# Performance work log

Hardware: AMD Instinct MI355X
Metric: run time of the kernel (lower is better)

The kernel has to match this reference:

```python
import jax, jax.numpy as jnp
import numpy as np

B, N_O, N_Q = 2, 512, 512
POS_DIM, LATENT, HEADS, HEAD_DIM, OUT_DIM = 3, 256, 8, 32, 128
HD = HEADS * HEAD_DIM  # == LATENT here


def _lin(key, fan_in, fan_out):
    return jax.random.normal(key, (fan_in, fan_out), jnp.float32) / np.sqrt(fan_in)


def setup_inputs() -> dict:
    key = jax.random.key(0)
    ks = jax.random.split(key, 12)
    return {
        'h_obs': jax.random.normal(ks[0], (B, N_O, LATENT), jnp.float32),
        'pos_obs': jax.random.uniform(ks[1], (B, N_O, POS_DIM), jnp.float32),
        'pos_query': jax.random.uniform(ks[2], (B, N_Q, POS_DIM), jnp.float32),
        'fw1': _lin(ks[3], LATENT, LATENT), 'fb1': jnp.zeros((LATENT,), jnp.float32),
        'fw2': _lin(ks[4], LATENT, HD), 'fb2': jnp.zeros((HD,), jnp.float32),
        'log_sigma': jnp.zeros((HEADS,), jnp.float32),
        'kw1': _lin(ks[5], POS_DIM * 3, LATENT), 'kb1': jnp.zeros((LATENT,), jnp.float32),
        'kw2': _lin(ks[6], LATENT, HEADS), 'kb2': jnp.zeros((HEADS,), jnp.float32),
        'ow': _lin(ks[7], HD, OUT_DIM), 'ob': jnp.zeros((OUT_DIM,), jnp.float32),
        'vw': _lin(ks[8], HD, OUT_DIM), 'vb': jnp.zeros((OUT_DIM,), jnp.float32),
    }


def reference(h_obs, pos_obs, pos_query, fw1, fb1, fw2, fb2, log_sigma,
              kw1, kb1, kw2, kb2, ow, ob, vw, vb):
    Bv, No, _ = h_obs.shape
    Nq = pos_query.shape[1]
    # feature net -> values [B, H, N_o, D]
    v = jax.nn.relu(h_obs @ fw1 + fb1) @ fw2 + fb2
    v = v.reshape(Bv, No, HEADS, HEAD_DIM).transpose(0, 2, 1, 3)
    # pairwise relative positions [B, Nq, No, P]
    pos_q = pos_query[:, :, None, :]
    pos_o = pos_obs[:, None, :, :]
    rel = pos_q - pos_o
    dist2 = jnp.sum(rel ** 2, axis=-1)  # [B, Nq, No]
    sigma = jnp.exp(log_sigma)[None, :, None, None]
    rbf = jnp.exp(-dist2[:, None] / (sigma ** 2 + 1e-6))  # [B, H, Nq, No]
    # kernel MLP on concatenated pairwise positions [B, Nq, No, 3P] -> [B, H, Nq, No]
    ki = jnp.concatenate([
        jnp.broadcast_to(pos_q, (Bv, Nq, No, POS_DIM)),
        jnp.broadcast_to(pos_o, (Bv, Nq, No, POS_DIM)),
        rel], axis=-1)
    delta = (jax.nn.relu(ki @ kw1 + kb1) @ kw2 + kb2).transpose(0, 3, 1, 2)
    logits = jnp.log(rbf + 1e-8) + delta
    weights = jax.nn.softmax(logits, axis=-1)  # [B, H, Nq, No]
    # weighted mean over observations
    v_mean = jnp.einsum('bhqo,bhod->bhqd', weights, v)  # [B, H, Nq, D]
    h_query = v_mean.transpose(0, 2, 1, 3).reshape(Bv, Nq, HD)
    # weighted variance: sum_o w * (v_o - v_mean)^2
    residual = v[:, :, None, :, :] - v_mean[:, :, :, None, :]  # [B, H, Nq, No, D]
    var = jnp.sum(weights[..., None] * residual ** 2, axis=3)  # [B, H, Nq, D]
    var = var.transpose(0, 2, 1, 3).reshape(Bv, Nq, HD)
    mean = h_query @ ow + ob
    var_out = jax.nn.softplus(var @ vw + vb)
    return (mean, var_out)
```

## Files before the change

### kernel.cpp

```cpp
#include <hip/hip_runtime.h>
#include <math.h>

#define NB 2
#define NO 512
#define NQ 512
#define OUT_DIM 128
#define LPAD 516

typedef __attribute__((ext_vector_type(8))) _Float16 half8;
typedef __attribute__((ext_vector_type(4))) _Float16 half4;
typedef __attribute__((ext_vector_type(4))) float f32x4;

__device__ __forceinline__ float softplus_f(float x) {
  return x > 0.0f ? x + log1pf(expf(-x)) : log1pf(expf(x));
}
__device__ __forceinline__ half8 splat8(_Float16 v) {
  return (half8){v, v, v, v, v, v, v, v};
}
__device__ __forceinline__ half8 fma8(half8 a, half8 b, half8 c) {
  return __builtin_elementwise_fma(a, b, c);
}
__device__ __forceinline__ half8 max8(half8 a, half8 b) {
  return __builtin_elementwise_max(a, b);
}
__device__ __forceinline__ void gll16(const void* g, void* l) {
  __builtin_amdgcn_global_load_lds(
      (const __attribute__((address_space(1))) unsigned int*)g,
      (__attribute__((address_space(3))) unsigned int*)l, 16, 0, 0);
}

__global__ __launch_bounds__(1024) void prep_kernel(
    const float* __restrict__ h_obs, const float* __restrict__ fw1,
    const float* __restrict__ fb1, const float* __restrict__ fw2,
    const float* __restrict__ fb2, _Float16* __restrict__ VT)
{
  __shared__ float s_red[4][4][256];
  __shared__ float s_hid[4][256];
  const int n  = threadIdx.x & 255;
  const int ks = threadIdx.x >> 8;
  const int r0 = blockIdx.x * 4;
  const int k0 = ks * 64;
  float a0 = 0.f, a1 = 0.f, a2 = 0.f, a3 = 0.f;
  #pragma unroll 8
  for (int kk = 0; kk < 64; ++kk) {
    int k = k0 + kk;
    float w = fw1[k * 256 + n];
    a0 = fmaf(h_obs[(r0 + 0) * 256 + k], w, a0);
    a1 = fmaf(h_obs[(r0 + 1) * 256 + k], w, a1);
    a2 = fmaf(h_obs[(r0 + 2) * 256 + k], w, a2);
    a3 = fmaf(h_obs[(r0 + 3) * 256 + k], w, a3);
  }
  s_red[ks][0][n] = a0; s_red[ks][1][n] = a1;
  s_red[ks][2][n] = a2; s_red[ks][3][n] = a3;
  __syncthreads();
  if (ks == 0) {
    float bb = fb1[n];
    #pragma unroll
    for (int r = 0; r < 4; ++r) {
      float v = s_red[0][r][n] + s_red[1][r][n] + s_red[2][r][n] + s_red[3][r][n] + bb;
      s_hid[r][n] = fmaxf(v, 0.f);
    }
  }
  __syncthreads();
  float c0 = 0.f, c1 = 0.f, c2 = 0.f, c3 = 0.f;
  #pragma unroll 8
  for (int kk = 0; kk < 64; ++kk) {
    int k = k0 + kk;
    float w = fw2[k * 256 + n];
    c0 = fmaf(s_hid[0][k], w, c0);
    c1 = fmaf(s_hid[1][k], w, c1);
    c2 = fmaf(s_hid[2][k], w, c2);
    c3 = fmaf(s_hid[3][k], w, c3);
  }
  __syncthreads();
  s_red[ks][0][n] = c0; s_red[ks][1][n] = c1;
  s_red[ks][2][n] = c2; s_red[ks][3][n] = c3;
  __syncthreads();
  if (ks == 0) {
    float bb = fb2[n];
    float vr[4];
    #pragma unroll
    for (int r = 0; r < 4; ++r)
      vr[r] = s_red[0][r][n] + s_red[1][r][n] + s_red[2][r][n] + s_red[3][r][n] + bb;
    const int h  = n >> 5, d = n & 31;
    const int bb_ = r0 >> 9, o0 = r0 & 511;
    half4 pv;
    #pragma unroll
    for (int r = 0; r < 4; ++r) pv[r] = (_Float16)vr[r];
    *(half4*)(VT + ((size_t)((bb_ * 8 + h) * 32 + d)) * 512 + o0) = pv;
  }
}

__global__ __launch_bounds__(512, 4) void attn_fused(
    const _Float16* __restrict__ VT,
    const float* __restrict__ kw1,
    const float* __restrict__ kb1,
    const float* __restrict__ kw2,
    const float* __restrict__ kb2,
    const float* __restrict__ log_sigma,
    const float* __restrict__ pos_obs,
    const float* __restrict__ pos_query,
    const float* __restrict__ ow, const float* __restrict__ obias,
    const float* __restrict__ vw, const float* __restrict__ vbias,
    float* __restrict__ out)
{
  __shared__ __align__(16) float s_logits[2][8 * LPAD];
  __shared__ __align__(16) _Float16 s_P16[2][8][520];
  __shared__ half8 s_Bh[512];
  __shared__ __align__(16) float s_pool[2048];
  __shared__ __align__(16) float s_po[3][516];
  __shared__ __align__(16) _Float16 s_co[3][264];

  _Float16* s_aq2 = (_Float16*)s_pool;
  float*    s_hv   = s_pool;
  float*    s_pred = s_pool + 1024;

  const int t   = threadIdx.x;
  const int bq0 = blockIdx.x * 2;
  const int b   = bq0 >> 9;

  float pqx[2], pqy[2], pqz[2];
  #pragma unroll
  for (int q = 0; q < 2; ++q) {
    pqx[q] = pos_query[(bq0 + q) * 3 + 0];
    pqy[q] = pos_query[(bq0 + q) * 3 + 1];
    pqz[q] = pos_query[(bq0 + q) * 3 + 2];
  }
  {
    const int q = t >> 8, j = t & 255;
    float c0 = kw1[0 * 256 + j] + kw1[6 * 256 + j];
    float c1 = kw1[1 * 256 + j] + kw1[7 * 256 + j];
    float c2 = kw1[2 * 256 + j] + kw1[8 * 256 + j];
    s_aq2[q * 256 + j] = (_Float16)
        fmaf(pqx[q], c0, fmaf(pqy[q], c1, fmaf(pqz[q], c2, kb1[j])));
  }
  if (t < 256) {
    const int j = t;
    s_co[0][j] = (_Float16)(kw1[3 * 256 + j] - kw1[6 * 256 + j]);
    s_co[1][j] = (_Float16)(kw1[4 * 256 + j] - kw1[7 * 256 + j]);
    s_co[2][j] = (_Float16)(kw1[5 * 256 + j] - kw1[8 * 256 + j]);
  }
  {
    const int o = t;
    const float* p = pos_obs + (size_t)(b * NO + o) * 3;
    float px = p[0], py = p[1], pz = p[2];
    s_po[0][o] = px; s_po[1][o] = py; s_po[2][o] = pz;
    float d2q[2];
    #pragma unroll
    for (int q = 0; q < 2; ++q) {
      float r0 = pqx[q] - px, r1 = pqy[q] - py, r2 = pqz[q] - pz;
      d2q[q] = r0 * r0 + r1 * r1 + r2 * r2;
    }
    #pragma unroll
    for (int h = 0; h < 8; ++h) {
      float sg  = __expf(log_sigma[h]);
      float inv = 1.0f / (sg * sg + 1e-6f);
      float kbv = kb2[h];
      s_logits[0][h * LPAD + o] = __logf(__expf(-d2q[0] * inv) + 1e-8f) + kbv;
      s_logits[1][h * LPAD + o] = __logf(__expf(-d2q[1] * inv) + 1e-8f) + kbv;
    }
  }
  {
    const int kstep = t >> 6, lane = t & 63;
    const int nh = lane & 15;
    const int kb_ = kstep * 32 + ((lane >> 4) & 3) * 8;
    half8 b8;
    #pragma unroll
    for (int i = 0; i < 8; ++i) {
      float v = (nh < 8) ? kw2[(kb_ + i) * 8 + nh] : 0.f;
      b8[i] = (_Float16)v;
    }
    s_Bh[kstep * 64 + lane] = b8;
  }
  __syncthreads();

  {
    const int wave = t >> 6, lane = t & 63;
    const int quad = lane >> 4, mrow = lane & 15;
    const int tb   = wave * 4;
    _Float16 pxh[4], pyh[4], pzh[4];
    #pragma unroll
    for (int jt = 0; jt < 4; ++jt) {
      const int o = (tb + jt) * 16 + mrow;
      pxh[jt] = (_Float16)s_po[0][o];
      pyh[jt] = (_Float16)s_po[1][o];
      pzh[jt] = (_Float16)s_po[2][o];
    }
    f32x4 C[2][4];
    #pragma unroll
    for (int q = 0; q < 2; ++q)
      #pragma unroll
      for (int jt = 0; jt < 4; ++jt) C[q][jt] = (f32x4){0.f, 0.f, 0.f, 0.f};

    const half8 z8 = {0, 0, 0, 0, 0, 0, 0, 0};
    #pragma unroll
    for (int kstep = 0; kstep < 8; ++kstep) {
      const int koff = kstep * 32 + quad * 8;
      half8 c0 = *(const half8*)&s_co[0][koff];
      half8 c1 = *(const half8*)&s_co[1][koff];
      half8 c2 = *(const half8*)&s_co[2][koff];
      half8 aq0 = *(const half8*)(s_aq2 + koff);
      half8 aq1 = *(const half8*)(s_aq2 + 256 + koff);
      half8 bh  = s_Bh[kstep * 64 + lane];
      #pragma unroll
      for (int jt = 0; jt < 4; ++jt) {
        half8 ao = fma8(splat8(pxh[jt]), c0,
                   fma8(splat8(pyh[jt]), c1, splat8(pzh[jt]) * c2));
        half8 a0 = max8(aq0 + ao, z8);
        half8 a1 = max8(aq1 + ao, z8);
        C[0][jt] = __builtin_amdgcn_mfma_f32_16x16x32_f16(a0, bh, C[0][jt], 0, 0, 0);
        C[1][jt] = __builtin_amdgcn_mfma_f32_16x16x32_f16(a1, bh, C[1][jt], 0, 0, 0);
      }
    }
    const int hh = lane & 15;
    if (hh < 8) {
      #pragma unroll
      for (int q = 0; q < 2; ++q)
        #pragma unroll
        for (int jt = 0; jt < 4; ++jt) {
          const int ob2 = (tb + jt) * 16 + quad * 4;
          #pragma unroll
          for (int r = 0; r < 4; ++r)
            s_logits[q][hh * LPAD + ob2 + r] += C[q][jt][r];
        }
    }
  }
  __syncthreads();

  {
    const int h = t >> 6, lane = t & 63;
    float invq[2];
    #pragma unroll
    for (int q = 0; q < 2; ++q) {
      float* pl = &s_logits[q][h * LPAD];
      float l8[8];
      float m = -1e30f;
      #pragma unroll
      for (int k = 0; k < 8; ++k) {
        l8[k] = pl[k * 64 + lane];
        m = fmaxf(m, l8[k]);
      }
      #pragma unroll
      for (int off = 32; off >= 1; off >>= 1) m = fmaxf(m, __shfl_xor(m, off, 64));
      float s = 0.f;
      #pragma unroll
      for (int k = 0; k < 8; ++k) {
        float p = __expf(l8[k] - m);
        s += p;
        s_P16[q][h][k * 64 + lane] = (_Float16)p;
      }
      #pragma unroll
      for (int off = 32; off >= 1; off >>= 1) s += __shfl_xor(s, off, 64);
      invq[q] = 1.0f / s;
    }
    __syncthreads();

    const int kg = lane >> 4, dl = lane & 15;
    char* stg = (char*)s_logits + h * 4096;
    const _Float16* vt = VT + ((size_t)(b * 8 + h) << 14);
    const _Float16* vsrc = vt + (lane >> 1) * 512 + (lane & 1) * 8;
    #define STAGE(j) gll16(vsrc + (j) * 16, stg + ((j) & 3) * 1024)
    STAGE(0); STAGE(1); STAGE(2); STAGE(3);

    const _Float16* pB = &s_P16[lane & 1][h][0];
    f32x4 Cm0 = {0.f, 0.f, 0.f, 0.f}, Cm1 = Cm0, Cv0 = Cm0, Cv1 = Cm0;
    #pragma unroll
    for (int ks = 0; ks < 16; ++ks) {
      if (ks < 15) asm volatile("s_waitcnt vmcnt(2)" ::: "memory");
      else         asm volatile("s_waitcnt vmcnt(0)" ::: "memory");
      const char* bufc = stg + ((2 * ks + (kg >> 1)) & 3) * 1024
                       + dl * 32 + (kg & 1) * 16;
      half8 am0 = *(const half8*)(bufc);
      half8 am1 = *(const half8*)(bufc + 512);
      half8 pb  = *(const half8*)(pB + ks * 32 + kg * 8);
      half8 av0 = am0 * am0;
      half8 av1 = am1 * am1;
      Cm0 = __builtin_amdgcn_mfma_f32_16x16x32_f16(am0, pb, Cm0, 0, 0, 0);
      Cm1 = __builtin_amdgcn_mfma_f32_16x16x32_f16(am1, pb, Cm1, 0, 0, 0);
      Cv0 = __builtin_amdgcn_mfma_f32_16x16x32_f16(av0, pb, Cv0, 0, 0, 0);
      Cv1 = __builtin_amdgcn_mfma_f32_16x16x32_f16(av1, pb, Cv1, 0, 0, 0);
      if (ks < 14) {
        asm volatile("s_waitcnt lgkmcnt(0)" ::: "memory");
        STAGE(2 * ks + 4); STAGE(2 * ks + 5);
      }
    }
    #undef STAGE
    const int nq = lane & 15;
    if (nq < 2) {
      const float iv = invq[nq];
      const int dbase = h * 32 + kg * 4;
      f32x4 m0, v0, m1, v1;
      #pragma unroll
      for (int r = 0; r < 4; ++r) {
        float a = Cm0[r] * iv;
        m0[r] = a; v0[r] = fmaxf(Cv0[r] * iv - a * a, 0.f);
        float c = Cm1[r] * iv;
        m1[r] = c; v1[r] = fmaxf(Cv1[r] * iv - c * c, 0.f);
      }
      *(f32x4*)(s_hv + (nq * 2 + 0) * 256 + dbase)      = m0;
      *(f32x4*)(s_hv + (nq * 2 + 1) * 256 + dbase)      = v0;
      *(f32x4*)(s_hv + (nq * 2 + 0) * 256 + dbase + 16) = m1;
      *(f32x4*)(s_hv + (nq * 2 + 1) * 256 + dbase + 16) = v1;
    }
  }
  __syncthreads();

  {
    const int ks = t >> 8, mode = (t >> 7) & 1, n = t & 127;
    const float* W  = mode ? vw : ow;
    const float* X0 = s_hv + mode * 256;
    const float* X1 = s_hv + (2 + mode) * 256;
    float a0 = 0.f, a1 = 0.f;
    const int k0 = ks * 128;
    #pragma unroll 4
    for (int k = k0; k < k0 + 128; k += 4) {
      float4 x0 = *(const float4*)&X0[k];
      float4 x1 = *(const float4*)&X1[k];
      float w0 = W[(k + 0) * 128 + n];
      float w1 = W[(k + 1) * 128 + n];
      float w2 = W[(k + 2) * 128 + n];
      float w3 = W[(k + 3) * 128 + n];
      a0 = fmaf(x0.x, w0, a0); a1 = fmaf(x1.x, w0, a1);
      a0 = fmaf(x0.y, w1, a0); a1 = fmaf(x1.y, w1, a1);
      a0 = fmaf(x0.z, w2, a0); a1 = fmaf(x1.z, w2, a1);
      a0 = fmaf(x0.w, w3, a0); a1 = fmaf(x1.w, w3, a1);
    }
    s_pred[((ks * 2 + mode) * 2 + 0) * 128 + n] = a0;
    s_pred[((ks * 2 + mode) * 2 + 1) * 128 + n] = a1;
  }
  __syncthreads();
  {
    const int q = t >> 8, mode = (t >> 7) & 1, n = t & 127;
    float v = s_pred[((0 * 2 + mode) * 2 + q) * 128 + n]
            + s_pred[((1 * 2 + mode) * 2 + q) * 128 + n]
            + (mode ? vbias[n] : obias[n]);
    if (mode) v = softplus_f(v);
    out[(size_t)mode * (NB * NQ * OUT_DIM) + (size_t)(bq0 + q) * OUT_DIM + n] = v;
  }
}

extern "C" void kernel_launch(void* const* d_in, const int* in_sizes, int n_in,
                              void* d_out, int out_size, void* d_ws, size_t ws_size,
                              hipStream_t stream)
{
  const float* h_obs     = (const float*)d_in[0];
  const float* pos_obs   = (const float*)d_in[1];
  const float* pos_query = (const float*)d_in[2];
  const float* fw1       = (const float*)d_in[3];
  const float* fb1       = (const float*)d_in[4];
  const float* fw2       = (const float*)d_in[5];
  const float* fb2       = (const float*)d_in[6];
  const float* log_sigma = (const float*)d_in[7];
  const float* kw1       = (const float*)d_in[8];
  const float* kb1       = (const float*)d_in[9];
  const float* kw2       = (const float*)d_in[10];
  const float* kb2       = (const float*)d_in[11];
  const float* ow        = (const float*)d_in[12];
  const float* ob        = (const float*)d_in[13];
  const float* vw        = (const float*)d_in[14];
  const float* vb        = (const float*)d_in[15];

  float* out = (float*)d_out;
  _Float16* VT = (_Float16*)d_ws;

  prep_kernel<<<256, 1024, 0, stream>>>(h_obs, fw1, fb1, fw2, fb2, VT);
  attn_fused<<<NB * NQ / 2, 512, 0, stream>>>(VT, kw1, kb1, kw2, kb2,
                                              log_sigma, pos_obs, pos_query,
                                              ow, ob, vw, vb, out);
}
```

Baseline: 127.7 us.

## Overlap V staging with softmax, drop barrier, simplify log-rbf

Replaces log(exp(x)+1e-8) with a clamp max(x, log(1e-8)), which removes two transcendentals per logit but is only an approximation near the clamp threshold. Starts the global-to-LDS staging of V before the softmax so the load overlaps with it, and removes the barrier between softmax and the MFMA loop by giving each wave its own staging buffers. The staging area moves out of the shared logits region into the wave's own logits rows and the s_Bh area. The softmax is interleaved across both queries, and the MFMA loop is split into even/odd halves with s_setprio raised around the MFMAs. The risk is a data race, because each wave now writes V tiles into logits rows and s_P16 entries that the barrier used to protect.

```diff
diff --git a/kernel.cpp b/kernel.cpp
--- a/kernel.cpp
+++ b/kernel.cpp
@@ -156,8 +156,8 @@
       float sg  = __expf(log_sigma[h]);
       float inv = 1.0f / (sg * sg + 1e-6f);
       float kbv = kb2[h];
-      s_logits[0][h * LPAD + o] = __logf(__expf(-d2q[0] * inv) + 1e-8f) + kbv;
-      s_logits[1][h * LPAD + o] = __logf(__expf(-d2q[1] * inv) + 1e-8f) + kbv;
+      s_logits[0][h * LPAD + o] = fmaxf(-d2q[0] * inv, -18.420681f) + kbv;
+      s_logits[1][h * LPAD + o] = fmaxf(-d2q[1] * inv, -18.420681f) + kbv;
     }
   }
   {
@@ -229,65 +229,104 @@
 
   {
     const int h = t >> 6, lane = t & 63;
-    float invq[2];
-    #pragma unroll
-    for (int q = 0; q < 2; ++q) {
-      float* pl = &s_logits[q][h * LPAD];
-      float l8[8];
-      float m = -1e30f;
+    const int kg = lane >> 4, dl = lane & 15;
+    char* stg0 = (char*)s_Bh + h * 1024;
+    char* b1   = (char*)&s_logits[0][h * LPAD];
+    char* b3   = b1 + 1024;
+    char* b2   = (char*)&s_logits[1][h * LPAD];
+    const _Float16* vsrc = VT + ((size_t)(b * 8 + h) << 14)
+                         + (lane >> 1) * 512 + (lane & 1) * 8;
+    gll16(vsrc, stg0);
+
+    float invq0, invq1;
+    {
+      const float* pl0 = &s_logits[0][h * LPAD];
+      const float* pl1 = &s_logits[1][h * LPAD];
+      float l0[8], l1[8];
+      float m0 = -1e30f, m1 = -1e30f;
       #pragma unroll
       for (int k = 0; k < 8; ++k) {
-        l8[k] = pl[k * 64 + lane];
-        m = fmaxf(m, l8[k]);
-      }
-      #pragma unroll
-      for (int off = 32; off >= 1; off >>= 1) m = fmaxf(m, __shfl_xor(m, off, 64));
-      float s = 0.f;
+        l0[k] = pl0[k * 64 + lane];
+        l1[k] = pl1[k * 64 + lane];
+        m0 = fmaxf(m0, l0[k]);
+        m1 = fmaxf(m1, l1[k]);
+      }
+      #pragma unroll
+      for (int off = 32; off >= 1; off >>= 1) {
+        m0 = fmaxf(m0, __shfl_xor(m0, off, 64));
+        m1 = fmaxf(m1, __shfl_xor(m1, off, 64));
+      }
+      float s0 = 0.f, s1 = 0.f;
+      _Float16* pp0 = &s_P16[0][h][0];
+      _Float16* pp1 = &s_P16[1][h][0];
       #pragma unroll
       for (int k = 0; k < 8; ++k) {
-        float p = __expf(l8[k] - m);
-        s += p;
-        s_P16[q][h][k * 64 + lane] = (_Float16)p;
-      }
-      #pragma unroll
-      for (int off = 32; off >= 1; off >>= 1) s += __shfl_xor(s, off, 64);
-      invq[q] = 1.0f / s;
-    }
-    __syncthreads();
-
-    const int kg = lane >> 4, dl = lane & 15;
-    char* stg = (char*)s_logits + h * 4096;
-    const _Float16* vt = VT + ((size_t)(b * 8 + h) << 14);
-    const _Float16* vsrc = vt + (lane >> 1) * 512 + (lane & 1) * 8;
-    #define STAGE(j) gll16(vsrc + (j) * 16, stg + ((j) & 3) * 1024)
-    STAGE(0); STAGE(1); STAGE(2); STAGE(3);
-
+        float p0 = __expf(l0[k] - m0);
+        float p1 = __expf(l1[k] - m1);
+        s0 += p0; s1 += p1;
+        pp0[k * 64 + lane] = (_Float16)p0;
+        pp1[k * 64 + lane] = (_Float16)p1;
+      }
+      #pragma unroll
+      for (int off = 32; off >= 1; off >>= 1) {
+        s0 += __shfl_xor(s0, off, 64);
+        s1 += __shfl_xor(s1, off, 64);
+      }
+      invq0 = 1.0f / s0; invq1 = 1.0f / s1;
+    }
+    gll16(vsrc + 16, b1);
+    gll16(vsrc + 32, b2);
+    gll16(vsrc + 48, b3);
+
+    const char* pE = ((kg & 2) ? b1 : stg0) + dl * 32 + (kg & 1) * 16;
+    const char* pO = ((kg & 2) ? b3 : b2)   + dl * 32 + (kg & 1) * 16;
     const _Float16* pB = &s_P16[lane & 1][h][0];
     f32x4 Cm0 = {0.f, 0.f, 0.f, 0.f}, Cm1 = Cm0, Cv0 = Cm0, Cv1 = Cm0;
     #pragma unroll
-    for (int ks = 0; ks < 16; ++ks) {
-      if (ks < 15) asm volatile("s_waitcnt vmcnt(2)" ::: "memory");
-      else         asm volatile("s_waitcnt vmcnt(0)" ::: "memory");
-      const char* bufc = stg + ((2 * ks + (kg >> 1)) & 3) * 1024
-                       + dl * 32 + (kg & 1) * 16;
-      half8 am0 = *(const half8*)(bufc);
-      half8 am1 = *(const half8*)(bufc + 512);
-      half8 pb  = *(const half8*)(pB + ks * 32 + kg * 8);
-      half8 av0 = am0 * am0;
-      half8 av1 = am1 * am1;
-      Cm0 = __builtin_amdgcn_mfma_f32_16x16x32_f16(am0, pb, Cm0, 0, 0, 0);
-      Cm1 = __builtin_amdgcn_mfma_f32_16x16x32_f16(am1, pb, Cm1, 0, 0, 0);
-      Cv0 = __builtin_amdgcn_mfma_f32_16x16x32_f16(av0, pb, Cv0, 0, 0, 0);
-      Cv1 = __builtin_amdgcn_mfma_f32_16x16x32_f16(av1, pb, Cv1, 0, 0, 0);
-      if (ks < 14) {
+    for (int kp = 0; kp < 8; ++kp) {
+      asm volatile("s_waitcnt vmcnt(2)" ::: "memory");
+      {
+        half8 am0 = *(const half8*)(pE);
+        half8 am1 = *(const half8*)(pE + 512);
+        half8 pb  = *(const half8*)(pB + (2 * kp) * 32 + kg * 8);
+        half8 av0 = am0 * am0;
+        half8 av1 = am1 * am1;
+        __builtin_amdgcn_s_setprio(1);
+        Cm0 = __builtin_amdgcn_mfma_f32_16x16x32_f16(am0, pb, Cm0, 0, 0, 0);
+        Cm1 = __builtin_amdgcn_mfma_f32_16x16x32_f16(am1, pb, Cm1, 0, 0, 0);
+        Cv0 = __builtin_amdgcn_mfma_f32_16x16x32_f16(av0, pb, Cv0, 0, 0, 0);
+        Cv1 = __builtin_amdgcn_mfma_f32_16x16x32_f16(av1, pb, Cv1, 0, 0, 0);
+        __builtin_amdgcn_s_setprio(0);
+      }
+      if (kp < 7) {
         asm volatile("s_waitcnt lgkmcnt(0)" ::: "memory");
-        STAGE(2 * ks + 4); STAGE(2 * ks + 5);
-      }
-    }
-    #undef STAGE
+        gll16(vsrc + (4 * kp + 4) * 16, stg0);
+        gll16(vsrc + (4 * kp + 5) * 16, b1);
+      }
+      if (kp < 7) asm volatile("s_waitcnt vmcnt(2)" ::: "memory");
+      else        asm volatile("s_waitcnt vmcnt(0)" ::: "memory");
+      {
+        half8 am0 = *(const half8*)(pO);
+        half8 am1 = *(const half8*)(pO + 512);
+        half8 pb  = *(const half8*)(pB + (2 * kp + 1) * 32 + kg * 8);
+        half8 av0 = am0 * am0;
+        half8 av1 = am1 * am1;
+        __builtin_amdgcn_s_setprio(1);
+        Cm0 = __builtin_amdgcn_mfma_f32_16x16x32_f16(am0, pb, Cm0, 0, 0, 0);
+        Cm1 = __builtin_amdgcn_mfma_f32_16x16x32_f16(am1, pb, Cm1, 0, 0, 0);
+        Cv0 = __builtin_amdgcn_mfma_f32_16x16x32_f16(av0, pb, Cv0, 0, 0, 0);
+        Cv1 = __builtin_amdgcn_mfma_f32_16x16x32_f16(av1, pb, Cv1, 0, 0, 0);
+        __builtin_amdgcn_s_setprio(0);
+      }
+      if (kp < 7) {
+        asm volatile("s_waitcnt lgkmcnt(0)" ::: "memory");
+        gll16(vsrc + (4 * kp + 6) * 16, b2);
+        gll16(vsrc + (4 * kp + 7) * 16, b3);
+      }
+    }
     const int nq = lane & 15;
     if (nq < 2) {
-      const float iv = invq[nq];
+      const float iv = nq ? invq1 : invq0;
       const int dbase = h * 32 + kg * 4;
       f32x4 m0, v0, m1, v1;
       #pragma unroll
```

Result: no change. 125.3 us (-1.9%).
